# Performance work log

Measured on AMD Instinct MI355X. Metric: run time of the kernel, lower is better.

Reference implementation:

```python
import jax, jax.numpy as jnp
import numpy as np

HEAD_DIM = 64
N_HEADS = 16


def _rope_tables(seq_len, head_dim):
    pos = np.arange(seq_len, dtype=np.float32)
    freq = np.arange(0, head_dim, 2, dtype=np.float32) / head_dim
    inv_freq = 1.0 / (10000.0 ** freq)
    angles = np.outer(pos, inv_freq)                     # [S, D/2]
    angles = np.repeat(angles, 2, axis=-1)               # [S, D] interleaved
    return jnp.asarray(np.cos(angles)), jnp.asarray(np.sin(angles))


def _rotate_half(x):
    x1 = x[..., ::2]
    x2 = x[..., 1::2]
    return jnp.stack((-x2, x1), axis=-1).reshape(x.shape)


def _apply_rope(x, cos, sin):
    # x: [B, H, S, D]; cos/sin: [S, D]
    return x * cos + _rotate_half(x) * sin


def setup_inputs() -> dict:
    key = jax.random.key(0)
    ks = jax.random.split(key, 5)
    d = N_HEADS * HEAD_DIM
    B, S = 4, 2048
    s = 1.0 / np.sqrt(d)
    return {
        "x": jax.random.normal(ks[0], (B, S, d), dtype=jnp.float32),
        "Wq": jax.random.normal(ks[1], (d, d), dtype=jnp.float32) * s,
        "bq": jnp.zeros((d,), jnp.float32),
        "Wk": jax.random.normal(ks[2], (d, d), dtype=jnp.float32) * s,
        "bk": jnp.zeros((d,), jnp.float32),
        "Wv": jax.random.normal(ks[3], (d, d), dtype=jnp.float32) * s,
        "bv": jnp.zeros((d,), jnp.float32),
        "Wo": jax.random.normal(ks[4], (d, d), dtype=jnp.float32) * s,
        "bo": jnp.zeros((d,), jnp.float32),
    }


def reference(x, Wq, bq, Wk, bk, Wv, bv, Wo, bo):
    B, S, d = x.shape
    H, D = N_HEADS, HEAD_DIM
    scale = D ** -0.5

    q = (x @ Wq + bq).reshape(B, S, H, D).transpose(0, 2, 1, 3)  # [B,H,S,D]
    k = (x @ Wk + bk).reshape(B, S, H, D).transpose(0, 2, 1, 3)
    v = (x @ Wv + bv).reshape(B, S, H, D).transpose(0, 2, 1, 3)

    cos, sin = _rope_tables(S, D)
    q = _apply_rope(q, cos, sin)
    k = _apply_rope(k, cos, sin)

    att = jnp.einsum("bhqd,bhkd->bhqk", q, k) * scale            # [B,H,S,S]
    causal = jnp.tril(jnp.ones((S, S), dtype=bool))
    att = jnp.where(causal, att, -jnp.inf)
    att = jax.nn.softmax(att, axis=-1)

    y = jnp.einsum("bhqk,bhkd->bhqd", att, v)                    # [B,H,S,D]
    y = y.transpose(0, 2, 1, 3).reshape(B, S, d)
    return y @ Wo + bo
```

## Files before the change

### kernel.cpp

```cpp
#include <hip/hip_runtime.h>

typedef __bf16 bf16;
typedef __bf16 bf16x2 __attribute__((ext_vector_type(2)));
typedef __bf16 bf16x8 __attribute__((ext_vector_type(8)));
typedef float  f32x4  __attribute__((ext_vector_type(4)));

#define MFMA16(a,b,c) __builtin_amdgcn_mfma_f32_16x16x32_bf16(a,b,c,0,0,0)
#define GLL16(g, l) __builtin_amdgcn_global_load_lds( \
    (const __attribute__((address_space(1))) unsigned char*)(g), \
    (__attribute__((address_space(3))) unsigned char*)(l), 16, 0, 0)

constexpr int SEQ   = 2048;
constexpr int NH    = 16;
constexpr int HD    = 64;
constexpr int BATCH = 4;
constexpr int DM    = 1024;
constexpr int ROWS  = BATCH * SEQ;
constexpr size_t TEN = (size_t)BATCH * NH * SEQ * HD;

__global__ __launch_bounds__(256) void k_convert_x(const float* __restrict__ x,
                                                   bf16* __restrict__ xb) {
    size_t idx = ((size_t)blockIdx.x * 256 + threadIdx.x) * 8;
    float4 f0 = *(const float4*)(x + idx);
    float4 f1 = *(const float4*)(x + idx + 4);
    bf16x8 o;
    o[0] = (bf16)f0.x; o[1] = (bf16)f0.y; o[2] = (bf16)f0.z; o[3] = (bf16)f0.w;
    o[4] = (bf16)f1.x; o[5] = (bf16)f1.y; o[6] = (bf16)f1.z; o[7] = (bf16)f1.w;
    *(bf16x8*)(xb + idx) = o;
}

__global__ __launch_bounds__(256) void k_wtrans(const float* __restrict__ W0,
                                                const float* __restrict__ W1,
                                                const float* __restrict__ W2,
                                                const float* __restrict__ W3,
                                                bf16* __restrict__ Wt_all) {
    __shared__ float T[64][65];
    const int z = blockIdx.z;
    const float* W = (z == 0) ? W0 : (z == 1) ? W1 : (z == 2) ? W2 : W3;
    bf16* Wt = Wt_all + (size_t)z * DM * DM;
    const int t = threadIdx.x;
    const int kb = blockIdx.x, nb = blockIdx.y;
    const int rl = t >> 2, seg = t & 3;
    const float* src = W + (size_t)(kb * 64 + rl) * DM + nb * 64 + seg * 16;
#pragma unroll
    for (int j4 = 0; j4 < 4; j4++) {
        float4 f = *(const float4*)(src + j4 * 4);
        T[rl][seg * 16 + j4 * 4 + 0] = f.x;
        T[rl][seg * 16 + j4 * 4 + 1] = f.y;
        T[rl][seg * 16 + j4 * 4 + 2] = f.z;
        T[rl][seg * 16 + j4 * 4 + 3] = f.w;
    }
    __syncthreads();
    bf16* dst = Wt + (size_t)(nb * 64 + rl) * DM + kb * 64 + seg * 16;
    bf16x8 o0, o1;
#pragma unroll
    for (int j = 0; j < 8; j++) {
        o0[j] = (bf16)T[seg * 16 + j][rl];
        o1[j] = (bf16)T[seg * 16 + 8 + j][rl];
    }
    *(bf16x8*)dst = o0;
    *(bf16x8*)(dst + 8) = o1;
}

template <int MODE>
__global__ __launch_bounds__(256) void k_gemm(const bf16* __restrict__ A,
                                              const bf16* __restrict__ Wt0,
                                              const float* __restrict__ b0,
                                              const float* __restrict__ b1,
                                              const float* __restrict__ b2,
                                              void* __restrict__ out) {
    __shared__ __align__(1024) bf16 AsF[128 * 32];
    __shared__ __align__(1024) bf16 BsF[128 * 32];
    const int z = blockIdx.z;
    const bf16* Wt = Wt0 + (size_t)z * DM * DM;
    const float* bias = (z == 0) ? b0 : (z == 1) ? b1 : b2;

    const int t = threadIdx.x;
    const int w = t >> 6, lane = t & 63, quad = lane >> 4, l16 = lane & 15;
    const int bm = blockIdx.x * 128, bn = blockIdx.y * 128;
    const int wm = (w >> 1) * 64, wn = (w & 1) * 64;

    const int c0 = w * 2, c1 = w * 2 + 1;
    const int sg0 = c0 * 64 + lane, sg1 = c1 * 64 + lane;
    const int r0 = sg0 >> 2, r1 = sg1 >> 2;
    const int csg0 = (sg0 & 3) ^ ((r0 >> 1) & 3);
    const int csg1 = (sg1 & 3) ^ ((r1 >> 1) & 3);
    const bf16* gA0 = A  + (size_t)(bm + r0) * DM + csg0 * 8;
    const bf16* gA1 = A  + (size_t)(bm + r1) * DM + csg1 * 8;
    const bf16* gB0 = Wt + (size_t)(bn + r0) * DM + csg0 * 8;
    const bf16* gB1 = Wt + (size_t)(bn + r1) * DM + csg1 * 8;
    bf16* lA0 = AsF + c0 * 512;
    bf16* lA1 = AsF + c1 * 512;
    bf16* lB0 = BsF + c0 * 512;
    bf16* lB1 = BsF + c1 * 512;

    const bf16* pA[4]; const bf16* pB[4];
#pragma unroll
    for (int mt = 0; mt < 4; mt++) {
        const int r = wm + mt * 16 + l16;
        pA[mt] = AsF + r * 32 + ((quad ^ ((r >> 1) & 3)) << 3);
    }
#pragma unroll
    for (int nt = 0; nt < 4; nt++) {
        const int r = wn + nt * 16 + l16;
        pB[nt] = BsF + r * 32 + ((quad ^ ((r >> 1) & 3)) << 3);
    }

    f32x4 zero = {0.f, 0.f, 0.f, 0.f};
    f32x4 acc[4][4];
#pragma unroll
    for (int mt = 0; mt < 4; mt++)
#pragma unroll
        for (int nt = 0; nt < 4; nt++) acc[mt][nt] = zero;

    for (int k0 = 0; k0 < DM; k0 += 32) {
        __syncthreads();
        GLL16(gA0, lA0);
        GLL16(gA1, lA1);
        GLL16(gB0, lB0);
        GLL16(gB1, lB1);
        gA0 += 32; gA1 += 32; gB0 += 32; gB1 += 32;
        __syncthreads();

        bf16x8 af[4], bfr[4];
#pragma unroll
        for (int mt = 0; mt < 4; mt++) af[mt]  = *(const bf16x8*)pA[mt];
#pragma unroll
        for (int nt = 0; nt < 4; nt++) bfr[nt] = *(const bf16x8*)pB[nt];
#pragma unroll
        for (int mt = 0; mt < 4; mt++)
#pragma unroll
            for (int nt = 0; nt < 4; nt++)
                acc[mt][nt] = MFMA16(af[mt], bfr[nt], acc[mt][nt]);
    }

    float bv[4];
#pragma unroll
    for (int nt = 0; nt < 4; nt++) bv[nt] = bias[bn + wn + nt * 16 + l16];

#pragma unroll
    for (int mt = 0; mt < 4; mt++) {
#pragma unroll
        for (int nt = 0; nt < 4; nt++) {
            const int col = bn + wn + nt * 16 + l16;
#pragma unroll
            for (int rg = 0; rg < 4; rg++) {
                const int row = bm + wm + mt * 16 + quad * 4 + rg;
                const float val = acc[mt][nt][rg] + bv[nt];
                if (MODE == 0) {
                    const int b = row >> 11, s = row & (SEQ - 1);
                    const int h = col >> 6, dd = col & 63;
                    ((bf16*)out)[(size_t)z * TEN +
                                 (((size_t)(b * NH + h)) * SEQ + s) * HD + dd] = (bf16)val;
                } else {
                    ((float*)out)[(size_t)row * DM + col] = val;
                }
            }
        }
    }
}

__global__ __launch_bounds__(256) void k_rope(bf16* __restrict__ q, bf16* __restrict__ k) {
    const int tid = blockIdx.x * 256 + threadIdx.x;
    const int i  = tid & 31;
    const int s  = (tid >> 5) & (SEQ - 1);
    const int bh = tid >> 16;
    const size_t base = ((size_t)bh * SEQ + s) * HD + 2 * i;
    const float inv_freq = expf(-(float)i * 0.28782313662425574f);
    const float ang = (float)s * inv_freq;
    float sn, cs;
    sincosf(ang, &sn, &cs);
    bf16x2 qv = *(bf16x2*)(q + base);
    bf16x2 kv = *(bf16x2*)(k + base);
    const float q0 = (float)qv[0], q1 = (float)qv[1];
    const float k0 = (float)kv[0], k1 = (float)kv[1];
    bf16x2 qo, ko;
    qo[0] = (bf16)((q0 * cs - q1 * sn) * 0.125f);
    qo[1] = (bf16)((q1 * cs + q0 * sn) * 0.125f);
    ko[0] = (bf16)(k0 * cs - k1 * sn);
    ko[1] = (bf16)(k1 * cs + k0 * sn);
    *(bf16x2*)(q + base) = qo;
    *(bf16x2*)(k + base) = ko;
}

__global__ __launch_bounds__(256) void k_vtrans(const bf16* __restrict__ v, bf16* __restrict__ vt) {
    __shared__ float T[64][65];
    const int t = threadIdx.x;
    const int sb = blockIdx.x, bh = blockIdx.y;
    const int rl = t >> 2, seg = t & 3;
    const bf16* src = v + ((size_t)bh * SEQ + sb * 64 + rl) * HD + seg * 16;
    bf16x8 i0 = *(const bf16x8*)src;
    bf16x8 i1 = *(const bf16x8*)(src + 8);
#pragma unroll
    for (int j = 0; j < 8; j++) {
        T[rl][seg * 16 + j]     = (float)i0[j];
        T[rl][seg * 16 + 8 + j] = (float)i1[j];
    }
    __syncthreads();
    bf16* dst = vt + ((size_t)bh * HD + rl) * SEQ + sb * 64 + seg * 16;
    bf16x8 o0, o1;
#pragma unroll
    for (int j = 0; j < 8; j++) {
        o0[j] = (bf16)T[seg * 16 + j][rl];
        o1[j] = (bf16)T[seg * 16 + 8 + j][rl];
    }
    *(bf16x8*)dst = o0;
    *(bf16x8*)(dst + 8) = o1;
}

__global__ __launch_bounds__(256, 2) void k_attn(const bf16* __restrict__ q,
                                                 const bf16* __restrict__ k,
                                                 const bf16* __restrict__ vt,
                                                 bf16* __restrict__ y) {
    __shared__ __align__(1024) bf16 KsF[64 * 64];
    __shared__ __align__(1024) bf16 VsF[64 * 64];
    __shared__ __align__(1024) bf16 PsF[4 * 32 * 64];
    const int t = threadIdx.x;
    const int w = t >> 6, lane = t & 63, quad = lane >> 4, l16 = lane & 15;
    const int bh = blockIdx.x;
    const int x  = blockIdx.y;
    const int b = bh >> 4, h = bh & 15;

    const int srow = lane >> 3;
    const int gseg = (lane & 7) ^ srow;
    const int c0 = w, c1 = w + 4;

    const bf16* kbase = k  + (size_t)bh * SEQ * HD;
    const bf16* vbase = vt + (size_t)bh * HD * SEQ;
    const float NEG_INF = -__builtin_inff();

    const bf16 *kf_p[4][2], *vf_p[4][2], *pf_p[2][2];
#pragma unroll
    for (int nt = 0; nt < 4; nt++) {
        const int r = nt * 16 + l16;
#pragma unroll
        for (int hh = 0; hh < 2; hh++) {
            const int sg = hh * 4 + quad;
            kf_p[nt][hh] = KsF + r * 64 + (((sg ^ (r & 7))) << 3);
            vf_p[nt][hh] = VsF + r * 64 + (((sg ^ (r & 7))) << 3);
        }
    }
#pragma unroll
    for (int mt = 0; mt < 2; mt++) {
        const int r = mt * 16 + l16;
#pragma unroll
        for (int hh = 0; hh < 2; hh++) {
            const int sg = hh * 4 + quad;
            pf_p[mt][hh] = PsF + w * 2048 + r * 64 + (((sg ^ (r & 7))) << 3);
        }
    }

#pragma unroll 1
    for (int pass = 0; pass < 2; pass++) {
        const int qb = pass ? x : 15 - x;

        bf16x8 qf[2][2];
#pragma unroll
        for (int mt = 0; mt < 2; mt++) {
            const bf16* qrow = q + ((size_t)bh * SEQ + qb * 128 + w * 32 + mt * 16 + l16) * HD;
            qf[mt][0] = *(const bf16x8*)(qrow + quad * 8);
            qf[mt][1] = *(const bf16x8*)(qrow + 32 + quad * 8);
        }

        f32x4 zero = {0.f, 0.f, 0.f, 0.f};
        f32x4 minus10 = {-10.f, -10.f, -10.f, -10.f};
        f32x4 acc_o[2][4];
        float l_acc[2][4];
#pragma unroll
        for (int mt = 0; mt < 2; mt++)
#pragma unroll
            for (int nt = 0; nt < 4; nt++) acc_o[mt][nt] = zero;
#pragma unroll
        for (int mt = 0; mt < 2; mt++)
#pragma unroll
            for (int rg = 0; rg < 4; rg++) l_acc[mt][rg] = 0.f;

        const bf16* kg0 = kbase + (size_t)(c0 * 8 + srow) * HD + gseg * 8;
        const bf16* kg1 = kbase + (size_t)(c1 * 8 + srow) * HD + gseg * 8;
        const bf16* vg0 = vbase + (size_t)(c0 * 8 + srow) * SEQ + gseg * 8;
        const bf16* vg1 = vbase + (size_t)(c1 * 8 + srow) * SEQ + gseg * 8;
        const int ktmax = 2 * qb + 1;

        for (int kt = 0; kt <= ktmax; kt++) {
            __syncthreads();
            GLL16(kg0, KsF + c0 * 512);
            GLL16(kg1, KsF + c1 * 512);
            GLL16(vg0, VsF + c0 * 512);
            GLL16(vg1, VsF + c1 * 512);
            kg0 += 64 * HD; kg1 += 64 * HD; vg0 += 64; vg1 += 64;
            __syncthreads();

            const int d = qb * 128 + w * 32 - kt * 64;
            if (d > -32) {
                f32x4 accs[2][4];
#pragma unroll
                for (int nt = 0; nt < 4; nt++) {
                    const bf16x8 kf0 = *(const bf16x8*)kf_p[nt][0];
                    const bf16x8 kf1 = *(const bf16x8*)kf_p[nt][1];
#pragma unroll
                    for (int mt = 0; mt < 2; mt++) {
                        f32x4 a = minus10;
                        a = MFMA16(qf[mt][0], kf0, a);
                        a = MFMA16(qf[mt][1], kf1, a);
                        accs[mt][nt] = a;
                    }
                }
                if (d < 64) {
#pragma unroll
                    for (int mt = 0; mt < 2; mt++) {
                        const int qr = d + mt * 16 + quad * 4;
#pragma unroll
                        for (int nt = 0; nt < 4; nt++) {
                            const int kv = nt * 16 + l16;
#pragma unroll
                            for (int rg = 0; rg < 4; rg++)
                                if (kv > qr + rg) accs[mt][nt][rg] = NEG_INF;
                        }
                    }
                }
#pragma unroll
                for (int mt = 0; mt < 2; mt++) {
#pragma unroll
                    for (int nt = 0; nt < 4; nt++) {
#pragma unroll
                        for (int rg = 0; rg < 4; rg++) {
                            const float p = __expf(accs[mt][nt][rg]);
                            l_acc[mt][rg] += p;
                            const int prow = mt * 16 + quad * 4 + rg;
                            const int psg  = (nt * 2 + (l16 >> 3)) ^ (prow & 7);
                            PsF[w * 2048 + prow * 64 + psg * 8 + (l16 & 7)] = (bf16)p;
                        }
                    }
                }
                bf16x8 pf[2][2];
#pragma unroll
                for (int mt = 0; mt < 2; mt++) {
                    pf[mt][0] = *(const bf16x8*)pf_p[mt][0];
                    pf[mt][1] = *(const bf16x8*)pf_p[mt][1];
                }
#pragma unroll
                for (int nt = 0; nt < 4; nt++) {
                    const bf16x8 vf0 = *(const bf16x8*)vf_p[nt][0];
                    const bf16x8 vf1 = *(const bf16x8*)vf_p[nt][1];
#pragma unroll
                    for (int mt = 0; mt < 2; mt++) {
                        acc_o[mt][nt] = MFMA16(pf[mt][0], vf0, acc_o[mt][nt]);
                        acc_o[mt][nt] = MFMA16(pf[mt][1], vf1, acc_o[mt][nt]);
                    }
                }
            }
        }

#pragma unroll
        for (int mt = 0; mt < 2; mt++) {
#pragma unroll
            for (int rg = 0; rg < 4; rg++) {
                float rs = l_acc[mt][rg];
                rs += __shfl_xor(rs, 1);
                rs += __shfl_xor(rs, 2);
                rs += __shfl_xor(rs, 4);
                rs += __shfl_xor(rs, 8);
                const float inv = 1.0f / rs;
                const int s = qb * 128 + w * 32 + mt * 16 + quad * 4 + rg;
#pragma unroll
                for (int nt = 0; nt < 4; nt++) {
                    const float val = acc_o[mt][nt][rg] * inv;
                    y[((size_t)(b * SEQ + s)) * DM + h * HD + nt * 16 + l16] = (bf16)val;
                }
            }
        }
    }
}

extern "C" void kernel_launch(void* const* d_in, const int* in_sizes, int n_in,
                              void* d_out, int out_size, void* d_ws, size_t ws_size,
                              hipStream_t stream) {
    const float* x  = (const float*)d_in[0];
    const float* Wq = (const float*)d_in[1];
    const float* bq = (const float*)d_in[2];
    const float* Wk = (const float*)d_in[3];
    const float* bk = (const float*)d_in[4];
    const float* Wv = (const float*)d_in[5];
    const float* bv = (const float*)d_in[6];
    const float* Wo = (const float*)d_in[7];
    const float* bo = (const float*)d_in[8];

    char* ws = (char*)d_ws;
    bf16* xb   = (bf16*)(ws);
    bf16* wall = (bf16*)(ws + (16ull << 20));
    bf16* qb   = (bf16*)(ws + (24ull << 20));
    bf16* kb   = (bf16*)(ws + (40ull << 20));
    bf16* vb   = (bf16*)(ws + (56ull << 20));
    bf16* vtb  = (bf16*)(ws + (72ull << 20));
    bf16* wot  = wall + 3ull * DM * DM;

    k_convert_x<<<4096, 256, 0, stream>>>(x, xb);
    k_wtrans<<<dim3(16, 16, 4), 256, 0, stream>>>(Wq, Wk, Wv, Wo, wall);
    k_gemm<0><<<dim3(64, 8, 3), 256, 0, stream>>>(xb, wall, bq, bk, bv, qb);
    k_rope<<<16384, 256, 0, stream>>>(qb, kb);
    k_vtrans<<<dim3(32, 64), 256, 0, stream>>>(vb, vtb);
    k_attn<<<dim3(64, 8), 256, 0, stream>>>(qb, kb, vtb, xb);
    k_gemm<1><<<dim3(64, 8, 1), 256, 0, stream>>>(xb, wot, bo, bo, bo, d_out);
}
```

Measured before the change: 266.7 us.

## Fuse RoPE into QKV GEMM epilogue, merge prep kernels, split attention passes

Merges the x conversion and weight transpose into one launch, applying the x conversion as an extra z-slice. RoPE and the q scaling move into the QKV GEMM epilogue, using a lane shuffle to fetch each pair partner, which removes the separate read-modify-write pass over Q and K. The attention kernel no longer runs two paired query blocks per workgroup; it launches one workgroup per query block (grid 64x16) and raises launch bounds to allow 4 blocks per CU. The trade-off is a loss of the explicit load balancing between long and short causal rows, plus a risk of register pressure under the tighter occupancy bound.

```diff
diff --git a/kernel.cpp b/kernel.cpp
--- a/kernel.cpp
+++ b/kernel.cpp
@@ -18,27 +18,32 @@
 constexpr int ROWS  = BATCH * SEQ;
 constexpr size_t TEN = (size_t)BATCH * NH * SEQ * HD;
 
-__global__ __launch_bounds__(256) void k_convert_x(const float* __restrict__ x,
-                                                   bf16* __restrict__ xb) {
-    size_t idx = ((size_t)blockIdx.x * 256 + threadIdx.x) * 8;
-    float4 f0 = *(const float4*)(x + idx);
-    float4 f1 = *(const float4*)(x + idx + 4);
-    bf16x8 o;
-    o[0] = (bf16)f0.x; o[1] = (bf16)f0.y; o[2] = (bf16)f0.z; o[3] = (bf16)f0.w;
-    o[4] = (bf16)f1.x; o[5] = (bf16)f1.y; o[6] = (bf16)f1.z; o[7] = (bf16)f1.w;
-    *(bf16x8*)(xb + idx) = o;
-}
-
-__global__ __launch_bounds__(256) void k_wtrans(const float* __restrict__ W0,
-                                                const float* __restrict__ W1,
-                                                const float* __restrict__ W2,
-                                                const float* __restrict__ W3,
-                                                bf16* __restrict__ Wt_all) {
+__global__ __launch_bounds__(256) void k_prep(const float* __restrict__ x,
+                                              const float* __restrict__ W0,
+                                              const float* __restrict__ W1,
+                                              const float* __restrict__ W2,
+                                              const float* __restrict__ W3,
+                                              bf16* __restrict__ Wt_all,
+                                              bf16* __restrict__ xb) {
     __shared__ float T[64][65];
     const int z = blockIdx.z;
+    const int t = threadIdx.x;
+    if (z == 4) {
+        const int bi = blockIdx.y * 16 + blockIdx.x;
+#pragma unroll
+        for (int c = 0; c < 16; c++) {
+            const size_t idx = (size_t)c * 524288 + ((size_t)bi * 256 + t) * 8;
+            float4 f0 = *(const float4*)(x + idx);
+            float4 f1 = *(const float4*)(x + idx + 4);
+            bf16x8 o;
+            o[0] = (bf16)f0.x; o[1] = (bf16)f0.y; o[2] = (bf16)f0.z; o[3] = (bf16)f0.w;
+            o[4] = (bf16)f1.x; o[5] = (bf16)f1.y; o[6] = (bf16)f1.z; o[7] = (bf16)f1.w;
+            *(bf16x8*)(xb + idx) = o;
+        }
+        return;
+    }
     const float* W = (z == 0) ? W0 : (z == 1) ? W1 : (z == 2) ? W2 : W3;
     bf16* Wt = Wt_all + (size_t)z * DM * DM;
-    const int t = threadIdx.x;
     const int kb = blockIdx.x, nb = blockIdx.y;
     const int rl = t >> 2, seg = t & 3;
     const float* src = W + (size_t)(kb * 64 + rl) * DM + nb * 64 + seg * 16;
@@ -134,9 +139,17 @@
                 acc[mt][nt] = MFMA16(af[mt], bfr[nt], acc[mt][nt]);
     }
 
-    float bv[4];
-#pragma unroll
-    for (int nt = 0; nt < 4; nt++) bv[nt] = bias[bn + wn + nt * 16 + l16];
+    float bv[4], invf[4];
+#pragma unroll
+    for (int nt = 0; nt < 4; nt++) {
+        const int col = bn + wn + nt * 16 + l16;
+        bv[nt] = bias[col];
+        if (MODE == 0) {
+            const int i = (col & 63) >> 1;
+            invf[nt] = __builtin_exp2f(-0.41524101186092029f * (float)i);
+        }
+    }
+    const int odd = l16 & 1;
 
 #pragma unroll
     for (int mt = 0; mt < 4; mt++) {
@@ -146,10 +159,18 @@
 #pragma unroll
             for (int rg = 0; rg < 4; rg++) {
                 const int row = bm + wm + mt * 16 + quad * 4 + rg;
-                const float val = acc[mt][nt][rg] + bv[nt];
+                float val = acc[mt][nt][rg] + bv[nt];
                 if (MODE == 0) {
                     const int b = row >> 11, s = row & (SEQ - 1);
                     const int h = col >> 6, dd = col & 63;
+                    if (z < 2) {
+                        const float partner = __shfl_xor(val, 1);
+                        float sn, cs;
+                        __sincosf((float)s * invf[nt], &sn, &cs);
+                        val = odd ? (val * cs + partner * sn)
+                                  : (val * cs - partner * sn);
+                        if (z == 0) val *= 0.125f;
+                    }
                     ((bf16*)out)[(size_t)z * TEN +
                                  (((size_t)(b * NH + h)) * SEQ + s) * HD + dd] = (bf16)val;
                 } else {
@@ -158,29 +179,6 @@
             }
         }
     }
-}
-
-__global__ __launch_bounds__(256) void k_rope(bf16* __restrict__ q, bf16* __restrict__ k) {
-    const int tid = blockIdx.x * 256 + threadIdx.x;
-    const int i  = tid & 31;
-    const int s  = (tid >> 5) & (SEQ - 1);
-    const int bh = tid >> 16;
-    const size_t base = ((size_t)bh * SEQ + s) * HD + 2 * i;
-    const float inv_freq = expf(-(float)i * 0.28782313662425574f);
-    const float ang = (float)s * inv_freq;
-    float sn, cs;
-    sincosf(ang, &sn, &cs);
-    bf16x2 qv = *(bf16x2*)(q + base);
-    bf16x2 kv = *(bf16x2*)(k + base);
-    const float q0 = (float)qv[0], q1 = (float)qv[1];
-    const float k0 = (float)kv[0], k1 = (float)kv[1];
-    bf16x2 qo, ko;
-    qo[0] = (bf16)((q0 * cs - q1 * sn) * 0.125f);
-    qo[1] = (bf16)((q1 * cs + q0 * sn) * 0.125f);
-    ko[0] = (bf16)(k0 * cs - k1 * sn);
-    ko[1] = (bf16)(k1 * cs + k0 * sn);
-    *(bf16x2*)(q + base) = qo;
-    *(bf16x2*)(k + base) = ko;
 }
 
 __global__ __launch_bounds__(256) void k_vtrans(const bf16* __restrict__ v, bf16* __restrict__ vt) {
@@ -208,7 +206,7 @@
     *(bf16x8*)(dst + 8) = o1;
 }
 
-__global__ __launch_bounds__(256, 2) void k_attn(const bf16* __restrict__ q,
+__global__ __launch_bounds__(256, 4) void k_attn(const bf16* __restrict__ q,
                                                  const bf16* __restrict__ k,
                                                  const bf16* __restrict__ vt,
                                                  bf16* __restrict__ y) {
@@ -218,7 +216,7 @@
     const int t = threadIdx.x;
     const int w = t >> 6, lane = t & 63, quad = lane >> 4, l16 = lane & 15;
     const int bh = blockIdx.x;
-    const int x  = blockIdx.y;
+    const int qb = 15 - (int)blockIdx.y;
     const int b = bh >> 4, h = bh & 15;
 
     const int srow = lane >> 3;
@@ -250,123 +248,118 @@
         }
     }
 
-#pragma unroll 1
-    for (int pass = 0; pass < 2; pass++) {
-        const int qb = pass ? x : 15 - x;
-
-        bf16x8 qf[2][2];
-#pragma unroll
-        for (int mt = 0; mt < 2; mt++) {
-            const bf16* qrow = q + ((size_t)bh * SEQ + qb * 128 + w * 32 + mt * 16 + l16) * HD;
-            qf[mt][0] = *(const bf16x8*)(qrow + quad * 8);
-            qf[mt][1] = *(const bf16x8*)(qrow + 32 + quad * 8);
-        }
-
-        f32x4 zero = {0.f, 0.f, 0.f, 0.f};
-        f32x4 minus10 = {-10.f, -10.f, -10.f, -10.f};
-        f32x4 acc_o[2][4];
-        float l_acc[2][4];
-#pragma unroll
-        for (int mt = 0; mt < 2; mt++)
-#pragma unroll
-            for (int nt = 0; nt < 4; nt++) acc_o[mt][nt] = zero;
-#pragma unroll
-        for (int mt = 0; mt < 2; mt++)
-#pragma unroll
-            for (int rg = 0; rg < 4; rg++) l_acc[mt][rg] = 0.f;
-
-        const bf16* kg0 = kbase + (size_t)(c0 * 8 + srow) * HD + gseg * 8;
-        const bf16* kg1 = kbase + (size_t)(c1 * 8 + srow) * HD + gseg * 8;
-        const bf16* vg0 = vbase + (size_t)(c0 * 8 + srow) * SEQ + gseg * 8;
-        const bf16* vg1 = vbase + (size_t)(c1 * 8 + srow) * SEQ + gseg * 8;
-        const int ktmax = 2 * qb + 1;
-
-        for (int kt = 0; kt <= ktmax; kt++) {
-            __syncthreads();
-            GLL16(kg0, KsF + c0 * 512);
-            GLL16(kg1, KsF + c1 * 512);
-            GLL16(vg0, VsF + c0 * 512);
-            GLL16(vg1, VsF + c1 * 512);
-            kg0 += 64 * HD; kg1 += 64 * HD; vg0 += 64; vg1 += 64;
-            __syncthreads();
-
-            const int d = qb * 128 + w * 32 - kt * 64;
-            if (d > -32) {
-                f32x4 accs[2][4];
+    bf16x8 qf[2][2];
+#pragma unroll
+    for (int mt = 0; mt < 2; mt++) {
+        const bf16* qrow = q + ((size_t)bh * SEQ + qb * 128 + w * 32 + mt * 16 + l16) * HD;
+        qf[mt][0] = *(const bf16x8*)(qrow + quad * 8);
+        qf[mt][1] = *(const bf16x8*)(qrow + 32 + quad * 8);
+    }
+
+    f32x4 zero = {0.f, 0.f, 0.f, 0.f};
+    f32x4 minus10 = {-10.f, -10.f, -10.f, -10.f};
+    f32x4 acc_o[2][4];
+    float l_acc[2][4];
+#pragma unroll
+    for (int mt = 0; mt < 2; mt++)
+#pragma unroll
+        for (int nt = 0; nt < 4; nt++) acc_o[mt][nt] = zero;
+#pragma unroll
+    for (int mt = 0; mt < 2; mt++)
+#pragma unroll
+        for (int rg = 0; rg < 4; rg++) l_acc[mt][rg] = 0.f;
+
+    const bf16* kg0 = kbase + (size_t)(c0 * 8 + srow) * HD + gseg * 8;
+    const bf16* kg1 = kbase + (size_t)(c1 * 8 + srow) * HD + gseg * 8;
+    const bf16* vg0 = vbase + (size_t)(c0 * 8 + srow) * SEQ + gseg * 8;
+    const bf16* vg1 = vbase + (size_t)(c1 * 8 + srow) * SEQ + gseg * 8;
+    const int ktmax = 2 * qb + 1;
+
+    for (int kt = 0; kt <= ktmax; kt++) {
+        __syncthreads();
+        GLL16(kg0, KsF + c0 * 512);
+        GLL16(kg1, KsF + c1 * 512);
+        GLL16(vg0, VsF + c0 * 512);
+        GLL16(vg1, VsF + c1 * 512);
+        kg0 += 64 * HD; kg1 += 64 * HD; vg0 += 64; vg1 += 64;
+        __syncthreads();
+
+        const int d = qb * 128 + w * 32 - kt * 64;
+        if (d > -32) {
+            f32x4 accs[2][4];
+#pragma unroll
+            for (int nt = 0; nt < 4; nt++) {
+                const bf16x8 kf0 = *(const bf16x8*)kf_p[nt][0];
+                const bf16x8 kf1 = *(const bf16x8*)kf_p[nt][1];
+#pragma unroll
+                for (int mt = 0; mt < 2; mt++) {
+                    f32x4 a = minus10;
+                    a = MFMA16(qf[mt][0], kf0, a);
+                    a = MFMA16(qf[mt][1], kf1, a);
+                    accs[mt][nt] = a;
+                }
+            }
+            if (d < 64) {
+#pragma unroll
+                for (int mt = 0; mt < 2; mt++) {
+                    const int qr = d + mt * 16 + quad * 4;
+#pragma unroll
+                    for (int nt = 0; nt < 4; nt++) {
+                        const int kv = nt * 16 + l16;
+#pragma unroll
+                        for (int rg = 0; rg < 4; rg++)
+                            if (kv > qr + rg) accs[mt][nt][rg] = NEG_INF;
+                    }
+                }
+            }
+#pragma unroll
+            for (int mt = 0; mt < 2; mt++) {
 #pragma unroll
                 for (int nt = 0; nt < 4; nt++) {
-                    const bf16x8 kf0 = *(const bf16x8*)kf_p[nt][0];
-                    const bf16x8 kf1 = *(const bf16x8*)kf_p[nt][1];
-#pragma unroll
-                    for (int mt = 0; mt < 2; mt++) {
-                        f32x4 a = minus10;
-                        a = MFMA16(qf[mt][0], kf0, a);
-                        a = MFMA16(qf[mt][1], kf1, a);
-                        accs[mt][nt] = a;
+#pragma unroll
+                    for (int rg = 0; rg < 4; rg++) {
+                        const float p = __expf(accs[mt][nt][rg]);
+                        l_acc[mt][rg] += p;
+                        const int prow = mt * 16 + quad * 4 + rg;
+                        const int psg  = (nt * 2 + (l16 >> 3)) ^ (prow & 7);
+                        PsF[w * 2048 + prow * 64 + psg * 8 + (l16 & 7)] = (bf16)p;
                     }
                 }
-                if (d < 64) {
-#pragma unroll
-                    for (int mt = 0; mt < 2; mt++) {
-                        const int qr = d + mt * 16 + quad * 4;
-#pragma unroll
-                        for (int nt = 0; nt < 4; nt++) {
-                            const int kv = nt * 16 + l16;
-#pragma unroll
-                            for (int rg = 0; rg < 4; rg++)
-                                if (kv > qr + rg) accs[mt][nt][rg] = NEG_INF;
-                        }
-                    }
-                }
+            }
+            bf16x8 pf[2][2];
+#pragma unroll
+            for (int mt = 0; mt < 2; mt++) {
+                pf[mt][0] = *(const bf16x8*)pf_p[mt][0];
+                pf[mt][1] = *(const bf16x8*)pf_p[mt][1];
+            }
+#pragma unroll
+            for (int nt = 0; nt < 4; nt++) {
+                const bf16x8 vf0 = *(const bf16x8*)vf_p[nt][0];
+                const bf16x8 vf1 = *(const bf16x8*)vf_p[nt][1];
 #pragma unroll
                 for (int mt = 0; mt < 2; mt++) {
-#pragma unroll
-                    for (int nt = 0; nt < 4; nt++) {
-#pragma unroll
-                        for (int rg = 0; rg < 4; rg++) {
-                            const float p = __expf(accs[mt][nt][rg]);
-                            l_acc[mt][rg] += p;
-                            const int prow = mt * 16 + quad * 4 + rg;
-                            const int psg  = (nt * 2 + (l16 >> 3)) ^ (prow & 7);
-                            PsF[w * 2048 + prow * 64 + psg * 8 + (l16 & 7)] = (bf16)p;
-                        }
-                    }
-                }
-                bf16x8 pf[2][2];
-#pragma unroll
-                for (int mt = 0; mt < 2; mt++) {
-                    pf[mt][0] = *(const bf16x8*)pf_p[mt][0];
-                    pf[mt][1] = *(const bf16x8*)pf_p[mt][1];
-                }
-#pragma unroll
-                for (int nt = 0; nt < 4; nt++) {
-                    const bf16x8 vf0 = *(const bf16x8*)vf_p[nt][0];
-                    const bf16x8 vf1 = *(const bf16x8*)vf_p[nt][1];
-#pragma unroll
-                    for (int mt = 0; mt < 2; mt++) {
-                        acc_o[mt][nt] = MFMA16(pf[mt][0], vf0, acc_o[mt][nt]);
-                        acc_o[mt][nt] = MFMA16(pf[mt][1], vf1, acc_o[mt][nt]);
-                    }
-                }
-            }
-        }
-
-#pragma unroll
-        for (int mt = 0; mt < 2; mt++) {
-#pragma unroll
-            for (int rg = 0; rg < 4; rg++) {
-                float rs = l_acc[mt][rg];
-                rs += __shfl_xor(rs, 1);
-                rs += __shfl_xor(rs, 2);
-                rs += __shfl_xor(rs, 4);
-                rs += __shfl_xor(rs, 8);
-                const float inv = 1.0f / rs;
-                const int s = qb * 128 + w * 32 + mt * 16 + quad * 4 + rg;
-#pragma unroll
-                for (int nt = 0; nt < 4; nt++) {
-                    const float val = acc_o[mt][nt][rg] * inv;
-                    y[((size_t)(b * SEQ + s)) * DM + h * HD + nt * 16 + l16] = (bf16)val;
-                }
+                    acc_o[mt][nt] = MFMA16(pf[mt][0], vf0, acc_o[mt][nt]);
+                    acc_o[mt][nt] = MFMA16(pf[mt][1], vf1, acc_o[mt][nt]);
+                }
+            }
+        }
+    }
+
+#pragma unroll
+    for (int mt = 0; mt < 2; mt++) {
+#pragma unroll
+        for (int rg = 0; rg < 4; rg++) {
+            float rs = l_acc[mt][rg];
+            rs += __shfl_xor(rs, 1);
+            rs += __shfl_xor(rs, 2);
+            rs += __shfl_xor(rs, 4);
+            rs += __shfl_xor(rs, 8);
+            const float inv = 1.0f / rs;
+            const int s = qb * 128 + w * 32 + mt * 16 + quad * 4 + rg;
+#pragma unroll
+            for (int nt = 0; nt < 4; nt++) {
+                const float val = acc_o[mt][nt][rg] * inv;
+                y[((size_t)(b * SEQ + s)) * DM + h * HD + nt * 16 + l16] = (bf16)val;
             }
         }
     }
@@ -394,11 +387,9 @@
     bf16* vtb  = (bf16*)(ws + (72ull << 20));
     bf16* wot  = wall + 3ull * DM * DM;
 
-    k_convert_x<<<4096, 256, 0, stream>>>(x, xb);
-    k_wtrans<<<dim3(16, 16, 4), 256, 0, stream>>>(Wq, Wk, Wv, Wo, wall);
+    k_prep<<<dim3(16, 16, 5), 256, 0, stream>>>(x, Wq, Wk, Wv, Wo, wall, xb);
     k_gemm<0><<<dim3(64, 8, 3), 256, 0, stream>>>(xb, wall, bq, bk, bv, qb);
-    k_rope<<<16384, 256, 0, stream>>>(qb, kb);
     k_vtrans<<<dim3(32, 64), 256, 0, stream>>>(vb, vtb);
-    k_attn<<<dim3(64, 8), 256, 0, stream>>>(qb, kb, vtb, xb);
+    k_attn<<<dim3(64, 16), 256, 0, stream>>>(qb, kb, vtb, xb);
     k_gemm<1><<<dim3(64, 8, 1), 256, 0, stream>>>(xb, wot, bo, bo, bo, d_out);
 }
```

After: 381.9 us. 43.2% more time.
